# Kernel optimization log

Hardware: AMD Instinct MI355X
Metric: run time of the kernel (lower is better)

The kernel has to match this reference:

```python
import jax, jax.numpy as jnp
import numpy as np

NEG = -1e9  # large negative instead of -inf for numerical safety; masked rows are zeroed afterwards
LN_EPS = 1e-5


def layer_norm(x, g, b):
    mu = jnp.mean(x, axis=-1, keepdims=True)
    var = jnp.mean(jnp.square(x - mu), axis=-1, keepdims=True)
    return (x - mu) * jax.lax.rsqrt(var + LN_EPS) * g + b


def causal_conv1d(x_bct, w_oik):
    # x: [B, C, T], w: [O, I, K]; left-pad by K-1 (causal ConvNorm)
    k = w_oik.shape[-1]
    return jax.lax.conv_general_dilated(
        x_bct, w_oik, window_strides=(1,), padding=[(k - 1, 0)],
        dimension_numbers=('NCH', 'OIH', 'NCH'))


def setup_inputs() -> dict:
    key = jax.random.key(0)
    ks = jax.random.split(key, 8)
    B, T, D, H, F, K = 2, 2048, 1024, 16, 4096, 3
    MAXLEN = 4096
    x = jax.random.normal(ks[0], (B, T, D), dtype=jnp.float32)
    lengths = jnp.array([2048, 1536])
    x_mask = jnp.arange(T)[None, :] >= lengths[:, None]  # True = padded
    std = 0.02
    pos_table = jax.random.normal(ks[1], (MAXLEN, D), dtype=jnp.float32) * std
    w_qkv = jax.random.normal(ks[2], (3 * D, D), dtype=jnp.float32) * std
    w_o = jax.random.normal(ks[3], (D, D), dtype=jnp.float32) * std
    conv1_w = jax.random.normal(ks[4], (F, D, K), dtype=jnp.float32) * std
    conv2_w = jax.random.normal(ks[5], (D, F, K), dtype=jnp.float32) * std
    return {
        'x': x, 'x_mask': x_mask, 'pos_table': pos_table,
        'w_qkv': w_qkv, 'w_o': w_o,
        'ln1_g': jnp.ones((D,)), 'ln1_b': jnp.zeros((D,)),
        'ln2_g': jnp.ones((D,)), 'ln2_b': jnp.zeros((D,)),
        'conv1_w': conv1_w, 'conv2_w': conv2_w,
    }


def reference(x, x_mask, pos_table, w_qkv, w_o, ln1_g, ln1_b, ln2_g, ln2_b, conv1_w, conv2_w):
    B, T, D = x.shape
    H = 16
    dh = D // H
    scale = dh ** -0.5

    # ---- self-attention block (pre-norm) ----
    q_in = layer_norm(x, ln1_g, ln1_b)
    q_in = q_in + pos_table[:T][None]  # learnable positional embeddings
    qkv = jnp.einsum('btd,ed->bte', q_in, w_qkv).reshape(B, T, 3, H, dh)
    q, k, v = qkv[:, :, 0], qkv[:, :, 1], qkv[:, :, 2]
    scores = jnp.einsum('bthd,bshd->bhts', q, k) * scale  # [B,H,T,T]
    pad_mask = x_mask[:, None, :, None]                    # mask padded query rows
    causal = jnp.tril(jnp.ones((T, T), dtype=bool))[None, None]
    scores = jnp.where(pad_mask | ~causal, NEG, scores)
    prob = jax.nn.softmax(scores, axis=-1)
    prob = jnp.where(pad_mask, 0.0, prob)
    y = jnp.einsum('bhts,bshd->bthd', prob, v).reshape(B, T, D)
    y = jnp.einsum('btd,ed->bte', y, w_o)
    x = x + y  # dropout p=0

    # ---- positionwise causal conv FFN (pre-norm) ----
    h = layer_norm(x, ln2_g, ln2_b)
    h = jnp.transpose(h, (0, 2, 1))           # [B, D, T]
    h = causal_conv1d(h, conv1_w)             # [B, F, T]
    h = jax.nn.gelu(h, approximate=True)
    h = causal_conv1d(h, conv2_w)             # [B, D, T]
    h = jnp.transpose(h, (0, 2, 1))
    x = x + h
    return x
```

## Files before the change

kernel.cpp:

```cpp
#include <hip/hip_runtime.h>
#include <stdint.h>
#include <math.h>

#define T_SEQ 2048
#define D_MODEL 1024
#define NHEAD 16
#define DH 64
#define F_FF 4096
#define TP (T_SEQ + 2)

typedef unsigned short u16;
typedef float f32x4 __attribute__((ext_vector_type(4)));
typedef __bf16 bf16x8 __attribute__((ext_vector_type(8)));

__device__ __forceinline__ u16 f2bf(float f){
  unsigned u = __float_as_uint(f);
  u = u + 0x7fffu + ((u >> 16) & 1u);
  return (u16)(u >> 16);
}
__device__ __forceinline__ float b2f(u16 h){ return __uint_as_float(((unsigned)h) << 16); }

__device__ __forceinline__ float gelu_f(float x){
  const float c = 0.7978845608028654f;
  float u = c * (x + 0.044715f * x * x * x);
  float e = __expf(-2.0f * u);
  return x * __builtin_amdgcn_rcpf(1.0f + e);
}

#define AS1 __attribute__((address_space(1)))
#define AS3 __attribute__((address_space(3)))
__device__ __forceinline__ void async_cp16(void* lds, const void* g){
  __builtin_amdgcn_global_load_lds((AS1 void*)(void*)g, (AS3 void*)lds, 16, 0, 0);
}

__device__ __forceinline__ float fload(const void* p, size_t i, unsigned isbf){
  return isbf ? b2f(((const u16*)p)[i]) : ((const float*)p)[i];
}

__global__ void detect_dtype(const u16* __restrict__ x, unsigned* __restrict__ flags){
  unsigned e = ((unsigned)x[threadIdx.x] >> 7) & 0xFF;
  bool good = (e == 0 || (e >= 90 && e <= 150));
  unsigned long long b = __ballot(good);
  if (threadIdx.x == 0) flags[0] = (b == ~0ULL) ? 1u : 0u;
}

__global__ __launch_bounds__(256) void canon_mask(const unsigned char* __restrict__ raw,
                                                  unsigned char* __restrict__ canon){
  int i = blockIdx.x * 256 + threadIdx.x;
  if (i >= 2 * T_SEQ) return;
  unsigned char v;
  if (raw[3584]) {
    v = raw[i] != 0;
  } else if (raw[7168]) {
    v = ((const u16*)raw)[i] != 0;
  } else if (raw[14336]) {
    v = ((const int*)raw)[i] != 0;
  } else {
    v = ((const long long*)raw)[i] != 0;
  }
  canon[i] = v;
}

__global__ __launch_bounds__(256)
void cast_any2bf(const void* __restrict__ in, u16* __restrict__ out, int n,
                 const unsigned* __restrict__ flags){
  int i = (blockIdx.x * 256 + threadIdx.x) * 4;
  if (i >= n) return;
  if (flags[0]){
    *(ushort4*)(out + i) = *(const ushort4*)((const u16*)in + i);
  } else {
    float4 v = *(const float4*)((const float*)in + i);
    ushort4 o = { f2bf(v.x), f2bf(v.y), f2bf(v.z), f2bf(v.w) };
    *(ushort4*)(out + i) = o;
  }
}

__global__ __launch_bounds__(256)
void cast_out(const float* __restrict__ in, const float* __restrict__ res,
              void* __restrict__ out, int n, const unsigned* __restrict__ flags){
  int i = (blockIdx.x * 256 + threadIdx.x) * 4;
  if (i >= n) return;
  float4 v = *(const float4*)(in + i);
  float4 r = *(const float4*)(res + i);
  v.x += r.x; v.y += r.y; v.z += r.z; v.w += r.w;
  if (flags[0]){
    ushort4 o = { f2bf(v.x), f2bf(v.y), f2bf(v.z), f2bf(v.w) };
    *(ushort4*)((u16*)out + i) = o;
  } else {
    *(float4*)((float*)out + i) = v;
  }
}

template<int INX1>
__global__ __launch_bounds__(256)
void ln_kernel(const void* __restrict__ inv, const void* __restrict__ g,
               const void* __restrict__ be, const void* __restrict__ pos,
               u16* __restrict__ out, int addpos, int padout,
               const unsigned* __restrict__ flags)
{
  const unsigned isbf = flags[0];
  const int r = blockIdx.x;
  const int bb = r >> 11, tt = r & (T_SEQ - 1);
  const size_t ib = (size_t)r * D_MODEL + threadIdx.x * 4;
  float v0, v1, v2, v3;
  if (INX1){
    float4 v = *(const float4*)((const float*)inv + ib);
    v0 = v.x; v1 = v.y; v2 = v.z; v3 = v.w;
  } else if (isbf){
    ushort4 u = *(const ushort4*)((const u16*)inv + ib);
    v0 = b2f(u.x); v1 = b2f(u.y); v2 = b2f(u.z); v3 = b2f(u.w);
  } else {
    float4 v = *(const float4*)((const float*)inv + ib);
    v0 = v.x; v1 = v.y; v2 = v.z; v3 = v.w;
  }
  float s  = v0 + v1 + v2 + v3;
  float s2 = v0*v0 + v1*v1 + v2*v2 + v3*v3;
  #pragma unroll
  for (int o = 1; o < 64; o <<= 1){ s += __shfl_xor(s, o); s2 += __shfl_xor(s2, o); }
  __shared__ float w1[4], w2[4];
  int w = threadIdx.x >> 6;
  if ((threadIdx.x & 63) == 0){ w1[w] = s; w2[w] = s2; }
  __syncthreads();
  float S  = w1[0] + w1[1] + w1[2] + w1[3];
  float S2 = w2[0] + w2[1] + w2[2] + w2[3];
  float mu  = S * (1.f / 1024.f);
  float var = S2 * (1.f / 1024.f) - mu * mu;
  float rs  = rsqrtf(var + 1e-5f);
  int d0 = threadIdx.x * 4;
  float o0 = (v0 - mu) * rs * fload(g, d0 + 0, isbf) + fload(be, d0 + 0, isbf);
  float o1 = (v1 - mu) * rs * fload(g, d0 + 1, isbf) + fload(be, d0 + 1, isbf);
  float o2 = (v2 - mu) * rs * fload(g, d0 + 2, isbf) + fload(be, d0 + 2, isbf);
  float o3 = (v3 - mu) * rs * fload(g, d0 + 3, isbf) + fload(be, d0 + 3, isbf);
  if (addpos){
    size_t pb = (size_t)tt * D_MODEL + d0;
    o0 += fload(pos, pb + 0, isbf);
    o1 += fload(pos, pb + 1, isbf);
    o2 += fload(pos, pb + 2, isbf);
    o3 += fload(pos, pb + 3, isbf);
  }
  size_t orow = padout ? ((size_t)bb * TP + tt + 2) * (size_t)D_MODEL
                       : (size_t)r * D_MODEL;
  ushort4 ov = { f2bf(o0), f2bf(o1), f2bf(o2), f2bf(o3) };
  *(ushort4*)(out + orow + d0) = ov;
}

__global__ __launch_bounds__(256)
void conv_w_split(const void* __restrict__ in, u16* __restrict__ out, int lg2C,
                  const unsigned* __restrict__ flags){
  int i = blockIdx.x * 256 + threadIdx.x;
  if (i >= 4096 * 1024) return;
  const unsigned isbf = flags[0];
  const int C = 1 << lg2C;
  int c = i & (C - 1);
  size_t sb = (size_t)i * 3;
  size_t ob = (size_t)(i >> lg2C) * 3 * C + c;
  out[ob]         = f2bf(fload(in, sb + 0, isbf));
  out[ob + C]     = f2bf(fload(in, sb + 1, isbf));
  out[ob + 2 * C] = f2bf(fload(in, sb + 2, isbf));
}

__global__ __launch_bounds__(256)
void zero_pads(u16* __restrict__ h2pad, u16* __restrict__ g1pad){
  int tid = blockIdx.x * 256 + threadIdx.x;
  if (tid < 2 * 2 * D_MODEL){
    int b = tid >> 11; int off = tid & (2 * D_MODEL - 1);
    h2pad[(size_t)b * TP * D_MODEL + off] = 0;
  }
  if (tid < 2 * 2 * F_FF){
    int b = tid >> 13; int off = tid & (2 * F_FF - 1);
    g1pad[(size_t)b * TP * F_FF + off] = 0;
  }
}

template<int MODE>
__global__ __launch_bounds__(256)
void gemm_bt(const u16* __restrict__ A, const u16* __restrict__ B,
             const void* __restrict__ res, void* __restrict__ outp,
             int N, int Kin, int lg2Kin, int nseg, long Abstride,
             const unsigned* __restrict__ flags)
{
  __shared__ u16 smA[128 * 32];
  __shared__ u16 smB[128 * 32];
  const int tid = threadIdx.x;
  const int m0 = blockIdx.y * 128;
  const int n0 = blockIdx.x * 128;
  const int Ktot = Kin * nseg;
  const int segz = (MODE == 4) ? blockIdx.z : 0;

  long abase[2]; const u16* bbase[2];
  #pragma unroll
  for (int i = 0; i < 2; ++i){
    int r = m0 + i * 64 + (tid >> 2);
    int bb = r >> 11, tt = r & (T_SEQ - 1);
    abase[i] = (long)bb * Abstride + (long)tt * Kin + (tid & 3) * 8;
    bbase[i] = B + (long)(n0 + i * 64 + (tid >> 2)) * Ktot + (tid & 3) * 8;
  }

  f32x4 acc[4][4];
  #pragma unroll
  for (int i = 0; i < 4; ++i)
    #pragma unroll
    for (int j = 0; j < 4; ++j){ f32x4 z = {0.f,0.f,0.f,0.f}; acc[i][j] = z; }

  const int wm = (tid >> 6) & 1, wn = (tid >> 7) & 1;
  const int lane = tid & 63, lq = lane >> 4, lr = lane & 15;
  const int aoff = (wm * 64 + lr) * 32 + lq * 8;
  const int boff = (wn * 64 + lr) * 32 + lq * 8;

  const int Kloop = (MODE == 4) ? Kin : Ktot;
  for (int k0 = 0; k0 < Kloop; k0 += 32){
    long aso, bso;
    if (MODE == 4){
      aso = (long)segz * Kin + k0;
      bso = aso;
    } else {
      int seg = k0 >> lg2Kin;
      int j0  = k0 & (Kin - 1);
      aso = (long)seg * Kin + j0;
      bso = k0;
    }
    #pragma unroll
    for (int i = 0; i < 2; ++i){
      async_cp16(&smA[i * 2048 + tid * 8], A + abase[i] + aso);
      async_cp16(&smB[i * 2048 + tid * 8], bbase[i] + bso);
    }
    __syncthreads();
    bf16x8 af[4], bfv[4];
    #pragma unroll
    for (int mi = 0; mi < 4; ++mi) af[mi]  = *(const bf16x8*)&smA[aoff + mi * 512];
    #pragma unroll
    for (int ni = 0; ni < 4; ++ni) bfv[ni] = *(const bf16x8*)&smB[boff + ni * 512];
    #pragma unroll
    for (int mi = 0; mi < 4; ++mi)
      #pragma unroll
      for (int ni = 0; ni < 4; ++ni)
        acc[mi][ni] = __builtin_amdgcn_mfma_f32_16x16x32_bf16(af[mi], bfv[ni], acc[mi][ni], 0, 0, 0);
    __syncthreads();
  }

  const unsigned isbf = (MODE == 1 || MODE == 3) ? flags[0] : 0;
  #pragma unroll
  for (int mi = 0; mi < 4; ++mi){
    #pragma unroll
    for (int ni = 0; ni < 4; ++ni){
      int row0 = m0 + wm * 64 + mi * 16 + lq * 4;
      int col  = n0 + wn * 64 + ni * 16 + lr;
      if (MODE == 0){
        ushort4 pv = { f2bf(acc[mi][ni][0]), f2bf(acc[mi][ni][1]),
                       f2bf(acc[mi][ni][2]), f2bf(acc[mi][ni][3]) };
        if (col < 2 * D_MODEL){
          #pragma unroll
          for (int rr = 0; rr < 4; ++rr)
            ((u16*)outp)[(size_t)(row0 + rr) * N + col] = ((const u16*)&pv)[rr];
        } else {
          int hh = (col - 2 * D_MODEL) >> 6, dd = (col - 2 * D_MODEL) & 63;
          int bb = row0 >> 11, tt = row0 & (T_SEQ - 1);
          *(ushort4*)((u16*)const_cast<void*>(res) +
                      ((size_t)(bb * NHEAD + hh) * 64 + dd) * T_SEQ + tt) = pv;
        }
      } else {
        #pragma unroll
        for (int rr = 0; rr < 4; ++rr){
          int row = row0 + rr;
          float v = acc[mi][ni][rr];
          size_t idx = (size_t)row * N + col;
          if (MODE == 1){
            ((float*)outp)[idx] = v + fload(res, idx, isbf);
          } else if (MODE == 2){
            int bb = row >> 11, tt = row & (T_SEQ - 1);
            ((u16*)outp)[((size_t)bb * TP + tt + 2) * N + col] = f2bf(gelu_f(v));
          } else if (MODE == 3){
            float ov = v + ((const float*)res)[idx];
            if (isbf) ((u16*)outp)[idx] = f2bf(ov);
            else      ((float*)outp)[idx] = ov;
          } else {
            atomicAdd((float*)outp + idx, v);
          }
        }
      }
    }
  }
}

__device__ __forceinline__ void ktile8(
    f32x4 (&acc)[8][4], u16 (*L)[16384], int buf, int abase, int bbase,
    const u16* __restrict__ A, const long (&asrc)[2], const u16* const (&bsrc)[2],
    const int (&adst)[2], const int (&bdst)[2], int kt, bool stage_ok)
{
  const u16* Lp = L[buf];
  bf16x8 bfr[4], a0[4];
  #pragma unroll
  for (int nf = 0; nf < 4; ++nf) bfr[nf] = *(const bf16x8*)&Lp[bbase + nf * 512];
  #pragma unroll
  for (int j = 0; j < 4; ++j) a0[j] = *(const bf16x8*)&Lp[abase + j * 512];
  if (stage_ok){
    u16* Ld = L[(kt + 3) & 3];
    #pragma unroll
    for (int s = 0; s < 2; ++s)
      async_cp16(&Ld[adst[s]], A + asrc[s] + (long)(kt + 3) * 32);
  }
  __builtin_amdgcn_s_barrier();
  __builtin_amdgcn_sched_barrier(0);
  __builtin_amdgcn_s_setprio(1);
  #pragma unroll
  for (int j = 0; j < 4; ++j)
    #pragma unroll
    for (int nf = 0; nf < 4; ++nf)
      acc[j][nf] = __builtin_amdgcn_mfma_f32_16x16x32_bf16(a0[j], bfr[nf], acc[j][nf], 0, 0, 0);
  __builtin_amdgcn_s_setprio(0);
  __builtin_amdgcn_s_barrier();
  __builtin_amdgcn_sched_barrier(0);
  bf16x8 a1[4];
  #pragma unroll
  for (int j = 0; j < 4; ++j) a1[j] = *(const bf16x8*)&Lp[abase + (4 + j) * 512];
  if (stage_ok){
    u16* Ld = L[(kt + 3) & 3];
    #pragma unroll
    for (int s = 0; s < 2; ++s)
      async_cp16(&Ld[bdst[s]], bsrc[s] + (long)(kt + 3) * 32);
  }
  __builtin_amdgcn_s_barrier();
  __builtin_amdgcn_sched_barrier(0);
  __builtin_amdgcn_s_setprio(1);
  #pragma unroll
  for (int j = 0; j < 4; ++j)
    #pragma unroll
    for (int nf = 0; nf < 4; ++nf)
      acc[4 + j][nf] = __builtin_amdgcn_mfma_f32_16x16x32_bf16(a1[j], bfr[nf], acc[4 + j][nf], 0, 0, 0);
  __builtin_amdgcn_s_setprio(0);
}

template<int MODE>
__global__ __launch_bounds__(512, 2)
void gemm8(const u16* __restrict__ A, const u16* __restrict__ Bm,
           u16* __restrict__ outp, int N, int Kin, int Ktot, long Abstride)
{
  __shared__ u16 L[4][16384];
  const int tid = threadIdx.x;
  const int m0 = blockIdx.y * 256, n0 = blockIdx.x * 256;
  const int NKT = Ktot >> 5;

  const int rl = tid >> 2;
  const int ch = (tid & 3) ^ (rl & 3);
  long asrc[2]; const u16* bsrc[2]; int adst[2], bdst[2];
  #pragma unroll
  for (int s = 0; s < 2; ++s){
    int r = m0 + s * 128 + rl;
    int bb = r >> 11, tt = r & (T_SEQ - 1);
    asrc[s] = (long)bb * Abstride + (long)tt * Kin + ch * 8;
    bsrc[s] = Bm + (long)(n0 + s * 128 + rl) * Ktot + ch * 8;
    adst[s] = (s * 512 + tid) * 8;
    bdst[s] = 8192 + adst[s];
  }

  const int w = tid >> 6, lane = tid & 63;
  const int wm = w >> 2, wn = w & 3;
  const int quad = lane >> 4, lr = lane & 15;
  const int xq = quad ^ (lr & 3);
  const int abase = ((wm * 128 + lr) * 4 + xq) * 8;
  const int bbase = 8192 + ((wn * 64 + lr) * 4 + xq) * 8;

  f32x4 acc[8][4];
  #pragma unroll
  for (int i = 0; i < 8; ++i)
    #pragma unroll
    for (int j = 0; j < 4; ++j){ f32x4 z = {0.f,0.f,0.f,0.f}; acc[i][j] = z; }

  #pragma unroll
  for (int j = 0; j < 3; ++j){
    #pragma unroll
    for (int s = 0; s < 2; ++s) async_cp16(&L[j][adst[s]], A + asrc[s] + j * 32);
    #pragma unroll
    for (int s = 0; s < 2; ++s) async_cp16(&L[j][bdst[s]], bsrc[s] + j * 32);
  }

  int kt = 0;
  for (; kt < NKT - 2; ++kt){
    asm volatile("s_waitcnt vmcnt(8)" ::: "memory");
    __builtin_amdgcn_s_barrier();
    __builtin_amdgcn_sched_barrier(0);
    ktile8(acc, L, kt & 3, abase, bbase, A, asrc, bsrc, adst, bdst, kt, kt + 3 < NKT);
  }
  asm volatile("s_waitcnt vmcnt(4)" ::: "memory");
  __builtin_amdgcn_s_barrier();
  __builtin_amdgcn_sched_barrier(0);
  ktile8(acc, L, (NKT - 2) & 3, abase, bbase, A, asrc, bsrc, adst, bdst, NKT - 2, false);
  asm volatile("s_waitcnt vmcnt(0)" ::: "memory");
  __builtin_amdgcn_s_barrier();
  __builtin_amdgcn_sched_barrier(0);
  ktile8(acc, L, (NKT - 1) & 3, abase, bbase, A, asrc, bsrc, adst, bdst, NKT - 1, false);

  #pragma unroll
  for (int mf = 0; mf < 8; ++mf){
    #pragma unroll
    for (int nf = 0; nf < 4; ++nf){
      int col = n0 + wn * 64 + nf * 16 + lr;
      #pragma unroll
      for (int rr = 0; rr < 4; ++rr){
        int row = m0 + wm * 128 + mf * 16 + quad * 4 + rr;
        int bb = row >> 11, tt = row & (T_SEQ - 1);
        outp[((size_t)(bb * TP + tt + 2)) * N + col] = f2bf(gelu_f(acc[mf][nf][rr]));
      }
    }
  }
}

__global__ __launch_bounds__(256)
void attn_mfma(const u16* __restrict__ qkv, const u16* __restrict__ vT,
               const unsigned char* __restrict__ mask, u16* __restrict__ y)
{
  const int qb = blockIdx.x, h = blockIdx.y, b = blockIdx.z;
  const int q0 = qb * 64;
  const int tid = threadIdx.x;

  if (mask[b * T_SEQ + q0]){
    int r = tid >> 2, c4 = (tid & 3) * 16;
    u16* yp = y + (size_t)(b * T_SEQ + q0 + r) * D_MODEL + h * DH + c4;
    ushort4 z = {0, 0, 0, 0};
    #pragma unroll
    for (int c = 0; c < 4; ++c) *(ushort4*)(yp + c * 4) = z;
    return;
  }

  const int w = tid >> 6, lane = tid & 63;
  const int quad = lane >> 4, lr = lane & 15;

  __shared__ u16 Ks[64 * 72];
  __shared__ u16 Vs[64 * 72];
  __shared__ u16 Ps[64 * 72];

  bf16x8 aq0, aq1;
  {
    const u16* qp = qkv + (size_t)(b * T_SEQ + q0 + w * 16 + lr) * 3072 + h * DH + quad * 8;
    aq0 = *(const bf16x8*)qp;
    aq1 = *(const bf16x8*)(qp + 32);
  }

  f32x4 acc_o[4];
  #pragma unroll
  for (int i = 0; i < 4; ++i){ f32x4 z = {0.f,0.f,0.f,0.f}; acc_o[i] = z; }
  float mrow[4] = {-1e30f, -1e30f, -1e30f, -1e30f};
  float lrow[4] = {0.f, 0.f, 0.f, 0.f};

  const int sr = tid >> 3, sg = tid & 7;

  for (int it = 0; it <= qb; ++it){
    const int s0 = it * 64;
    #pragma unroll
    for (int rr = 0; rr < 64; rr += 32){
      int row = sr + rr;
      *(uint4*)&Ks[row * 72 + sg * 8] =
        *(const uint4*)(qkv + (size_t)(b * T_SEQ + s0 + row) * 3072 + D_MODEL + h * DH + sg * 8);
      *(uint4*)&Vs[row * 72 + sg * 8] =
        *(const uint4*)(vT + ((size_t)(b * NHEAD + h) * 64 + row) * T_SEQ + s0 + sg * 8);
    }
    __syncthreads();

    f32x4 accs[4];
    #pragma unroll
    for (int nt = 0; nt < 4; ++nt){
      f32x4 z = {0.f, 0.f, 0.f, 0.f};
      bf16x8 bk0 = *(const bf16x8*)&Ks[(nt * 16 + lr) * 72 + quad * 8];
      bf16x8 bk1 = *(const bf16x8*)&Ks[(nt * 16 + lr) * 72 + quad * 8 + 32];
      z = __builtin_amdgcn_mfma_f32_16x16x32_bf16(aq0, bk0, z, 0, 0, 0);
      z = __builtin_amdgcn_mfma_f32_16x16x32_bf16(aq1, bk1, z, 0, 0, 0);
      accs[nt] = z;
    }

    const bool diag = (it == qb);
    float sv[4][4], mx[4];
    #pragma unroll
    for (int rr = 0; rr < 4; ++rr) mx[rr] = -1e30f;
    #pragma unroll
    for (int nt = 0; nt < 4; ++nt){
      #pragma unroll
      for (int rr = 0; rr < 4; ++rr){
        float s = accs[nt][rr] * 0.125f;
        if (diag && (nt * 16 + lr) > (w * 16 + quad * 4 + rr)) s = -1e30f;
        sv[nt][rr] = s;
        mx[rr] = fmaxf(mx[rr], s);
      }
    }
    #pragma unroll
    for (int o = 1; o < 16; o <<= 1){
      #pragma unroll
      for (int rr = 0; rr < 4; ++rr) mx[rr] = fmaxf(mx[rr], __shfl_xor(mx[rr], o));
    }
    float alpha[4], psum[4];
    #pragma unroll
    for (int rr = 0; rr < 4; ++rr){
      float mnew = fmaxf(mrow[rr], mx[rr]);
      alpha[rr] = __expf(mrow[rr] - mnew);
      mrow[rr] = mnew;
      psum[rr] = 0.f;
    }
    #pragma unroll
    for (int nt = 0; nt < 4; ++nt){
      #pragma unroll
      for (int rr = 0; rr < 4; ++rr){
        float p = __expf(sv[nt][rr] - mrow[rr]);
        psum[rr] += p;
        Ps[(w * 16 + quad * 4 + rr) * 72 + nt * 16 + lr] = f2bf(p);
      }
    }
    #pragma unroll
    for (int o = 1; o < 16; o <<= 1){
      #pragma unroll
      for (int rr = 0; rr < 4; ++rr) psum[rr] += __shfl_xor(psum[rr], o);
    }
    #pragma unroll
    for (int rr = 0; rr < 4; ++rr) lrow[rr] = lrow[rr] * alpha[rr] + psum[rr];
    #pragma unroll
    for (int nt = 0; nt < 4; ++nt)
      #pragma unroll
      for (int rr = 0; rr < 4; ++rr) acc_o[nt][rr] *= alpha[rr];

    bf16x8 ap0 = *(const bf16x8*)&Ps[(w * 16 + lr) * 72 + quad * 8];
    bf16x8 ap1 = *(const bf16x8*)&Ps[(w * 16 + lr) * 72 + quad * 8 + 32];
    #pragma unroll
    for (int nt = 0; nt < 4; ++nt){
      bf16x8 bv0 = *(const bf16x8*)&Vs[(nt * 16 + lr) * 72 + quad * 8];
      bf16x8 bv1 = *(const bf16x8*)&Vs[(nt * 16 + lr) * 72 + quad * 8 + 32];
      acc_o[nt] = __builtin_amdgcn_mfma_f32_16x16x32_bf16(ap0, bv0, acc_o[nt], 0, 0, 0);
      acc_o[nt] = __builtin_amdgcn_mfma_f32_16x16x32_bf16(ap1, bv1, acc_o[nt], 0, 0, 0);
    }
    __syncthreads();
  }

  #pragma unroll
  for (int rr = 0; rr < 4; ++rr){
    int qg = q0 + w * 16 + quad * 4 + rr;
    float inv = 1.0f / lrow[rr];
    bool rm = mask[b * T_SEQ + qg] != 0;
    #pragma unroll
    for (int nt = 0; nt < 4; ++nt){
      float v = rm ? 0.f : acc_o[nt][rr] * inv;
      y[(size_t)(b * T_SEQ + qg) * D_MODEL + h * DH + nt * 16 + lr] = f2bf(v);
    }
  }
}

extern "C" void kernel_launch(void* const* d_in, const int* in_sizes, int n_in,
                              void* d_out, int out_size, void* d_ws, size_t ws_size,
                              hipStream_t stream)
{
  const void* x       = d_in[0];
  const unsigned char* xmask_raw = (const unsigned char*)d_in[1];
  const void* pos     = d_in[2];
  const void* w_qkv   = d_in[3];
  const void* w_o     = d_in[4];
  const void* ln1_g   = d_in[5];
  const void* ln1_b   = d_in[6];
  const void* ln2_g   = d_in[7];
  const void* ln2_b   = d_in[8];
  const void* conv1_w = d_in[9];
  const void* conv2_w = d_in[10];

  char* ws = (char*)d_ws;
  size_t o = 0;
  auto alloc = [&](size_t bytes){ size_t cur = o; o += (bytes + 255) & ~(size_t)255; return cur; };
  unsigned* flags = (unsigned*)(ws + alloc(256));
  unsigned char* maskc = (unsigned char*)(ws + alloc(2 * T_SEQ));
  float* x1   = (float*)(ws + alloc((size_t)2 * T_SEQ * D_MODEL * 4));
  char* h2slab = ws + alloc((size_t)2 * TP * D_MODEL * 2);
  u16* g1pad  = (u16*)(ws + alloc((size_t)2 * TP * F_FF * 2));
  u16* slabA  = (u16*)(ws + alloc((size_t)4096 * 3072 * 2));
  u16* qy     = (u16*)(ws + alloc((size_t)4096 * 1024 * 2));
  char* vslab = ws + alloc((size_t)4096 * 1024 * 4);
  u16* vt     = (u16*)vslab;
  float* xc   = (float*)vslab;

  u16* wqkv_c = (u16*)h2slab;
  u16* wo_c   = (u16*)h2slab + (size_t)3072 * 1024;
  u16* h2pad  = (u16*)h2slab;
  u16* qin    = qy;
  u16* qkvb   = slabA;
  u16* yb     = qy;
  u16* W1cat  = slabA;
  u16* W2cat  = slabA;

  detect_dtype<<<1, 64, 0, stream>>>((const u16*)x, flags);
  canon_mask<<<16, 256, 0, stream>>>(xmask_raw, maskc);
  cast_any2bf<<<3072 * 1024 / 4 / 256, 256, 0, stream>>>(w_qkv, wqkv_c, 3072 * 1024, flags);
  cast_any2bf<<<1024 * 1024 / 4 / 256, 256, 0, stream>>>(w_o, wo_c, 1024 * 1024, flags);
  ln_kernel<0><<<4096, 256, 0, stream>>>(x, ln1_g, ln1_b, pos, qin, 1, 0, flags);
  gemm_bt<0><<<dim3(24, 32), 256, 0, stream>>>(qin, wqkv_c, vt, qkvb,
                                               3072, 1024, 10, 1, (long)T_SEQ * 1024, flags);
  attn_mfma<<<dim3(32, 16, 2), 256, 0, stream>>>(qkvb, vt, maskc, yb);
  gemm_bt<1><<<dim3(8, 32), 256, 0, stream>>>(yb, wo_c, x, x1,
                                              1024, 1024, 10, 1, (long)T_SEQ * 1024, flags);
  hipMemsetAsync(xc, 0, (size_t)4096 * 1024 * 4, stream);
  conv_w_split<<<4096 * 1024 / 256, 256, 0, stream>>>(conv1_w, W1cat, 10, flags);
  zero_pads<<<64, 256, 0, stream>>>(h2pad, g1pad);
  ln_kernel<1><<<4096, 256, 0, stream>>>(x1, ln2_g, ln2_b, nullptr, h2pad, 0, 1, flags);
  gemm8<2><<<dim3(16, 16), 512, 0, stream>>>(h2pad, W1cat, g1pad,
                                             4096, 1024, 3072, (long)TP * 1024);
  conv_w_split<<<4096 * 1024 / 256, 256, 0, stream>>>(conv2_w, W2cat, 12, flags);
  gemm_bt<4><<<dim3(8, 32, 3), 256, 0, stream>>>(g1pad, W2cat, nullptr, xc,
                                                 1024, 4096, 12, 3, (long)TP * 4096, flags);
  cast_out<<<4096 * 1024 / 4 / 256, 256, 0, stream>>>(xc, x1, d_out, 4096 * 1024, flags);
}
```

Baseline: 683.2 us.

## Run conv2 GEMM with the pipelined 256x256 gemm8 kernel using split-K atomics

Generalizes gemm8 with a k-tile range per z-block and an atomicAdd fp32 epilogue, then uses it for the second causal conv (K=12288 split four ways). This replaces the simpler 128x128 gemm_bt split-by-tap kernel, aiming for higher MFMA utilization through larger tiles and the multi-buffered async pipeline. The trade-offs are fewer blocks (256) and continued atomic accumulation into the fp32 buffer.

```diff
diff --git a/kernel.cpp b/kernel.cpp
--- a/kernel.cpp
+++ b/kernel.cpp
@@ -185,7 +185,6 @@
   const int m0 = blockIdx.y * 128;
   const int n0 = blockIdx.x * 128;
   const int Ktot = Kin * nseg;
-  const int segz = (MODE == 4) ? blockIdx.z : 0;
 
   long abase[2]; const u16* bbase[2];
   #pragma unroll
@@ -207,18 +206,11 @@
   const int aoff = (wm * 64 + lr) * 32 + lq * 8;
   const int boff = (wn * 64 + lr) * 32 + lq * 8;
 
-  const int Kloop = (MODE == 4) ? Kin : Ktot;
-  for (int k0 = 0; k0 < Kloop; k0 += 32){
-    long aso, bso;
-    if (MODE == 4){
-      aso = (long)segz * Kin + k0;
-      bso = aso;
-    } else {
-      int seg = k0 >> lg2Kin;
-      int j0  = k0 & (Kin - 1);
-      aso = (long)seg * Kin + j0;
-      bso = k0;
-    }
+  for (int k0 = 0; k0 < Ktot; k0 += 32){
+    int seg = k0 >> lg2Kin;
+    int j0  = k0 & (Kin - 1);
+    long aso = (long)seg * Kin + j0;
+    long bso = k0;
     #pragma unroll
     for (int i = 0; i < 2; ++i){
       async_cp16(&smA[i * 2048 + tid * 8], A + abase[i] + aso);
@@ -266,15 +258,10 @@
           size_t idx = (size_t)row * N + col;
           if (MODE == 1){
             ((float*)outp)[idx] = v + fload(res, idx, isbf);
-          } else if (MODE == 2){
-            int bb = row >> 11, tt = row & (T_SEQ - 1);
-            ((u16*)outp)[((size_t)bb * TP + tt + 2) * N + col] = f2bf(gelu_f(v));
           } else if (MODE == 3){
             float ov = v + ((const float*)res)[idx];
             if (isbf) ((u16*)outp)[idx] = f2bf(ov);
             else      ((float*)outp)[idx] = ov;
-          } else {
-            atomicAdd((float*)outp + idx, v);
           }
         }
       }
@@ -333,12 +320,13 @@
 template<int MODE>
 __global__ __launch_bounds__(512, 2)
 void gemm8(const u16* __restrict__ A, const u16* __restrict__ Bm,
-           u16* __restrict__ outp, int N, int Kin, int Ktot, long Abstride)
+           void* __restrict__ outp, int N, int Kin, int Ktot, int nkt, long Abstride)
 {
   __shared__ u16 L[4][16384];
   const int tid = threadIdx.x;
   const int m0 = blockIdx.y * 256, n0 = blockIdx.x * 256;
-  const int NKT = Ktot >> 5;
+  const int kt0 = (MODE == 4) ? blockIdx.z * nkt : 0;
+  const int ktEnd = kt0 + nkt;
 
   const int rl = tid >> 2;
   const int ch = (tid & 3) ^ (rl & 3);
@@ -369,26 +357,26 @@
   #pragma unroll
   for (int j = 0; j < 3; ++j){
     #pragma unroll
-    for (int s = 0; s < 2; ++s) async_cp16(&L[j][adst[s]], A + asrc[s] + j * 32);
-    #pragma unroll
-    for (int s = 0; s < 2; ++s) async_cp16(&L[j][bdst[s]], bsrc[s] + j * 32);
-  }
-
-  int kt = 0;
-  for (; kt < NKT - 2; ++kt){
+    for (int s = 0; s < 2; ++s) async_cp16(&L[(kt0 + j) & 3][adst[s]], A + asrc[s] + (long)(kt0 + j) * 32);
+    #pragma unroll
+    for (int s = 0; s < 2; ++s) async_cp16(&L[(kt0 + j) & 3][bdst[s]], bsrc[s] + (long)(kt0 + j) * 32);
+  }
+
+  int kt = kt0;
+  for (; kt < ktEnd - 2; ++kt){
     asm volatile("s_waitcnt vmcnt(8)" ::: "memory");
     __builtin_amdgcn_s_barrier();
     __builtin_amdgcn_sched_barrier(0);
-    ktile8(acc, L, kt & 3, abase, bbase, A, asrc, bsrc, adst, bdst, kt, kt + 3 < NKT);
+    ktile8(acc, L, kt & 3, abase, bbase, A, asrc, bsrc, adst, bdst, kt, kt + 3 < ktEnd);
   }
   asm volatile("s_waitcnt vmcnt(4)" ::: "memory");
   __builtin_amdgcn_s_barrier();
   __builtin_amdgcn_sched_barrier(0);
-  ktile8(acc, L, (NKT - 2) & 3, abase, bbase, A, asrc, bsrc, adst, bdst, NKT - 2, false);
+  ktile8(acc, L, (ktEnd - 2) & 3, abase, bbase, A, asrc, bsrc, adst, bdst, ktEnd - 2, false);
   asm volatile("s_waitcnt vmcnt(0)" ::: "memory");
   __builtin_amdgcn_s_barrier();
   __builtin_amdgcn_sched_barrier(0);
-  ktile8(acc, L, (NKT - 1) & 3, abase, bbase, A, asrc, bsrc, adst, bdst, NKT - 1, false);
+  ktile8(acc, L, (ktEnd - 1) & 3, abase, bbase, A, asrc, bsrc, adst, bdst, ktEnd - 1, false);
 
   #pragma unroll
   for (int mf = 0; mf < 8; ++mf){
@@ -398,8 +386,12 @@
       #pragma unroll
       for (int rr = 0; rr < 4; ++rr){
         int row = m0 + wm * 128 + mf * 16 + quad * 4 + rr;
-        int bb = row >> 11, tt = row & (T_SEQ - 1);
-        outp[((size_t)(bb * TP + tt + 2)) * N + col] = f2bf(gelu_f(acc[mf][nf][rr]));
+        if (MODE == 2){
+          int bb = row >> 11, tt = row & (T_SEQ - 1);
+          ((u16*)outp)[((size_t)(bb * TP + tt + 2)) * N + col] = f2bf(gelu_f(acc[mf][nf][rr]));
+        } else {
+          atomicAdd((float*)outp + (size_t)row * N + col, acc[mf][nf][rr]);
+        }
       }
     }
   }
@@ -593,10 +585,10 @@
   conv_w_split<<<4096 * 1024 / 256, 256, 0, stream>>>(conv1_w, W1cat, 10, flags);
   zero_pads<<<64, 256, 0, stream>>>(h2pad, g1pad);
   ln_kernel<1><<<4096, 256, 0, stream>>>(x1, ln2_g, ln2_b, nullptr, h2pad, 0, 1, flags);
-  gemm8<2><<<dim3(16, 16), 512, 0, stream>>>(h2pad, W1cat, g1pad,
-                                             4096, 1024, 3072, (long)TP * 1024);
+  gemm8<2><<<dim3(16, 16, 1), 512, 0, stream>>>(h2pad, W1cat, g1pad,
+                                                4096, 1024, 3072, 96, (long)TP * 1024);
   conv_w_split<<<4096 * 1024 / 256, 256, 0, stream>>>(conv2_w, W2cat, 12, flags);
-  gemm_bt<4><<<dim3(8, 32, 3), 256, 0, stream>>>(g1pad, W2cat, nullptr, xc,
-                                                 1024, 4096, 12, 3, (long)TP * 4096, flags);
+  gemm8<4><<<dim3(4, 16, 4), 512, 0, stream>>>(g1pad, W2cat, xc,
+                                               1024, 4096, 12288, 96, (long)TP * 4096);
   cast_out<<<4096 * 1024 / 4 / 256, 256, 0, stream>>>(xc, x1, d_out, 4096 * 1024, flags);
 }
```

Result: faster. 663.5 us (-2.9%).
